# Optimization experiments

Hardware: AMD Instinct MI355X
Metric: run time of the kernel (lower is better)

Reference implementation:

```python
import jax, jax.numpy as jnp
from jax import lax
import numpy as np

B, S, D, H = 64, 512, 1024, 1024


def setup_inputs() -> dict:
    key = jax.random.key(0)
    ks = jax.random.split(key, 9)
    s = 1.0 / np.sqrt(H)
    return {
        "x": jax.random.normal(ks[0], (B, S, D), jnp.float32),
        "W_ih0": jax.random.normal(ks[1], (H, D), jnp.float32) * s,
        "b_ih0": jax.random.normal(ks[2], (H,), jnp.float32) * s,
        "W_hh0": jax.random.normal(ks[3], (H, H), jnp.float32) * s,
        "b_hh0": jax.random.normal(ks[4], (H,), jnp.float32) * s,
        "W_ih1": jax.random.normal(ks[5], (H, H), jnp.float32) * s,
        "b_ih1": jax.random.normal(ks[6], (H,), jnp.float32) * s,
        "W_hh1": jax.random.normal(ks[7], (H, H), jnp.float32) * s,
        "b_hh1": jax.random.normal(ks[8], (H,), jnp.float32) * s,
    }


def reference(x, W_ih0, b_ih0, W_hh0, b_hh0, W_ih1, b_ih1, W_hh1, b_hh1):
    batch = x.shape[0]
    hid = W_hh0.shape[0]
    params = [(W_ih0, b_ih0, W_hh0, b_hh0), (W_ih1, b_ih1, W_hh1, b_hh1)]
    h0 = jnp.zeros((len(params), batch, hid), x.dtype)

    def step(h, xt):
        # xt: [B, D]; h: [L, B, H]
        inp = xt
        new_h = []
        for l, (Wi, bi, Wh, bh) in enumerate(params):
            inp = jnp.tanh(inp @ Wi.T + bi + h[l] @ Wh.T + bh)
            new_h.append(inp)
        return jnp.stack(new_h), inp

    hT, outs = lax.scan(step, h0, jnp.swapaxes(x, 0, 1))  # outs: [S, B, H]
    return jnp.swapaxes(outs, 0, 1), hT
```

## Files before the change

### kernel.cpp

```cpp
#include <hip/hip_runtime.h>
#include <hip/hip_bf16.h>

#define RNN_B 64
#define RNN_S 512
#define RNN_H 1024
#define BH (RNN_B * RNN_H)
#define L0_NBLK 64
#define L1_NBLK 128
#define NBLK (L0_NBLK + L1_NBLK)
#define NFLAGS 192
#define FLAG_STRIDE 32
#define OUTS_ELEMS ((size_t)RNN_B * RNN_S * RNN_H)

typedef _Float16 f16;
typedef __attribute__((ext_vector_type(8))) _Float16 f16x8;
typedef __attribute__((ext_vector_type(8))) short bf16x8;
typedef __attribute__((ext_vector_type(4))) float f32x4;
typedef __attribute__((ext_vector_type(2))) float f32x2;
typedef __attribute__((ext_vector_type(4))) int i32x4;

__device__ f32x4 __rnn_rawbufload_x4(i32x4 srsrc, int voffset, int soffset,
                                     int cachepolicy) __asm("llvm.amdgcn.raw.buffer.load.v4f32");

__device__ __forceinline__ i32x4 make_srd(const void* p, unsigned bytes) {
  i32x4 r;
  r[0] = (int)(unsigned)(unsigned long long)p;
  r[1] = (int)((unsigned long long)p >> 32);
  r[2] = (int)bytes;
  r[3] = 0x00020000;
  return r;
}

__device__ __forceinline__ f16x8 ld_h(i32x4 srd, int byteoff) {
  union { f32x4 f; f16x8 h; } u;
  u.f = __rnn_rawbufload_x4(srd, byteoff, 0, 17);
  return u.h;
}

__device__ __forceinline__ void st_sys_u32(void* p, unsigned v) {
  asm volatile("global_store_dword %0, %1, off sc0 sc1" :: "v"(p), "v"(v) : "memory");
}
__device__ __forceinline__ void st_sys_u64(void* p, unsigned long long v) {
  asm volatile("global_store_dwordx2 %0, %1, off sc0 sc1" :: "v"(p), "v"(v) : "memory");
}

__device__ __forceinline__ unsigned pack2f16(float a, float b) {
  union { f16 h[2]; unsigned u; } v;
  v.h[0] = (f16)a; v.h[1] = (f16)b;
  return v.u;
}
__device__ __forceinline__ unsigned long long pack4f16(const float* f) {
  union { f16 h[4]; unsigned long long u; } v;
  #pragma unroll
  for (int i = 0; i < 4; ++i) v.h[i] = (f16)f[i];
  return v.u;
}

__device__ __forceinline__ short f2bf(float f) {
  union { float f; unsigned u; } v; v.f = f;
  return (short)((v.u + 0x7FFFu + ((v.u >> 16) & 1u)) >> 16);
}
__device__ __forceinline__ float bf2f(short h) {
  union { unsigned u; float f; } v; v.u = ((unsigned)(unsigned short)h) << 16;
  return v.f;
}
__device__ __forceinline__ f32x4 mfma16b(bf16x8 a, bf16x8 b, f32x4 c) {
  return __builtin_amdgcn_mfma_f32_16x16x32_bf16(a, b, c, 0, 0, 0);
}
__device__ __forceinline__ f32x4 mfma16f(f16x8 a, f16x8 b, f32x4 c) {
  return __builtin_amdgcn_mfma_f32_16x16x32_f16(a, b, c, 0, 0, 0);
}
__device__ __forceinline__ void cvt8_hl(const float* f, bf16x8* hi, bf16x8* lo) {
  #pragma unroll
  for (int i = 0; i < 8; ++i) {
    short h = f2bf(f[i]);
    (*hi)[i] = h;
    (*lo)[i] = f2bf(f[i] - bf2f(h));
  }
}
__device__ __forceinline__ f16x8 cvt8f(const float* f) {
  f16x8 r;
  #pragma unroll
  for (int i = 0; i < 8; ++i) r[i] = (f16)f[i];
  return r;
}

__global__ __launch_bounds__(256) void a0_gemm(
    const float* __restrict__ x, const float* __restrict__ Wih0,
    const float* __restrict__ bih0, const float* __restrict__ bhh0,
    float* __restrict__ A0, unsigned* __restrict__ flags)
{
  if (blockIdx.x == 0) {
    for (int i = threadIdx.x; i < NFLAGS * FLAG_STRIDE; i += 256)
      __hip_atomic_store(&flags[i], 0u, __ATOMIC_RELAXED, __HIP_MEMORY_SCOPE_SYSTEM);
  }
  const int bn = blockIdx.x & 7;
  const int bm = blockIdx.x >> 3;
  const int tid = threadIdx.x;
  const int lane = tid & 63;
  const int w = tid >> 6;
  const int wr = w >> 1, wc = w & 1;
  const int l15 = lane & 15, lq = lane >> 4;

  __shared__ short As[2][128][40];
  __shared__ short Bs[2][128][40];

  f32x4 acc[4][4] = {};

  const int sr = tid >> 1;
  const int sc = (tid & 1) << 4;
  const float* xp = x + (size_t)(bm * 128 + sr) * RNN_H + sc;
  const float* wp = Wih0 + (size_t)(bn * 128 + sr) * RNN_H + sc;

  for (int k0 = 0; k0 < RNN_H; k0 += 32) {
    float xa[16], wa[16];
    #pragma unroll
    for (int j = 0; j < 4; ++j) {
      *(float4*)&xa[j * 4] = *(const float4*)(xp + k0 + j * 4);
      *(float4*)&wa[j * 4] = *(const float4*)(wp + k0 + j * 4);
    }
    __syncthreads();
    bf16x8 h0, l0, h1, l1;
    cvt8_hl(&xa[0], &h0, &l0); cvt8_hl(&xa[8], &h1, &l1);
    *(bf16x8*)&As[0][sr][sc] = h0; *(bf16x8*)&As[1][sr][sc] = l0;
    *(bf16x8*)&As[0][sr][sc + 8] = h1; *(bf16x8*)&As[1][sr][sc + 8] = l1;
    cvt8_hl(&wa[0], &h0, &l0); cvt8_hl(&wa[8], &h1, &l1);
    *(bf16x8*)&Bs[0][sr][sc] = h0; *(bf16x8*)&Bs[1][sr][sc] = l0;
    *(bf16x8*)&Bs[0][sr][sc + 8] = h1; *(bf16x8*)&Bs[1][sr][sc + 8] = l1;
    __syncthreads();
    bf16x8 ah[4], al[4], bh[4], bl[4];
    #pragma unroll
    for (int i = 0; i < 4; ++i) {
      ah[i] = *(const bf16x8*)&As[0][wr * 64 + i * 16 + l15][lq * 8];
      al[i] = *(const bf16x8*)&As[1][wr * 64 + i * 16 + l15][lq * 8];
    }
    #pragma unroll
    for (int j = 0; j < 4; ++j) {
      bh[j] = *(const bf16x8*)&Bs[0][wc * 64 + j * 16 + l15][lq * 8];
      bl[j] = *(const bf16x8*)&Bs[1][wc * 64 + j * 16 + l15][lq * 8];
    }
    #pragma unroll
    for (int i = 0; i < 4; ++i)
      #pragma unroll
      for (int j = 0; j < 4; ++j) {
        acc[i][j] = mfma16b(ah[i], bh[j], acc[i][j]);
        acc[i][j] = mfma16b(al[i], bh[j], acc[i][j]);
        acc[i][j] = mfma16b(ah[i], bl[j], acc[i][j]);
      }
  }

  #pragma unroll
  for (int j = 0; j < 4; ++j) {
    const int col = bn * 128 + wc * 64 + j * 16 + l15;
    const float bias = bih0[col] + bhh0[col];
    #pragma unroll
    for (int i = 0; i < 4; ++i) {
      const int row0 = bm * 128 + wr * 64 + i * 16 + lq * 4;
      #pragma unroll
      for (int r = 0; r < 4; ++r)
        A0[(size_t)(row0 + r) * RNN_H + col] = acc[i][j][r] + bias;
    }
  }
}

__device__ __forceinline__ void waitflags(const unsigned* fbase, int tL0, int tL1) {
  if (threadIdx.x < 64) {
    const int l = threadIdx.x;
    const unsigned* f = fbase + (l < 48 ? l : 0) * FLAG_STRIDE;
    const int tgt = (l < 16) ? tL0 : (l < 48 ? tL1 : (-0x7FFFFFFF));
    while (!__all((int)__hip_atomic_load(f, __ATOMIC_RELAXED,
                                         __HIP_MEMORY_SCOPE_SYSTEM) >= tgt))
      __builtin_amdgcn_s_sleep(1);
  }
  __syncthreads();
}

__device__ __forceinline__ void publish(unsigned* slot, unsigned v) {
  asm volatile("s_waitcnt vmcnt(0)" ::: "memory");
  __syncthreads();
  if (threadIdx.x == 0)
    __hip_atomic_store(slot, v, __ATOMIC_RELAXED, __HIP_MEMORY_SCOPE_SYSTEM);
}

__global__ __launch_bounds__(256) void rnn_rec(
    const float* __restrict__ Whh0,
    const float* __restrict__ Wih1, const float* __restrict__ bih1,
    const float* __restrict__ Whh1, const float* __restrict__ bhh1,
    float* outs,
    f16* __restrict__ h0buf,
    f16* __restrict__ h1buf,
    unsigned* flags, int dmask)
{
  const int bid = blockIdx.x;
  const bool isL0 = bid < L0_NBLK;
  const int tid = threadIdx.x;
  const int w = tid >> 6;
  const int lane = tid & 63;
  const int l15 = lane & 15;
  const int lq = lane >> 4;
  const int swz = l15 & 7;
  const int dlag = dmask;

  int b0, n0, bs, cs;
  if (isL0) { bs = bid >> 4; cs = bid & 15; b0 = bs * 16; n0 = cs * 64; }
  else { const int b2 = bid - L0_NBLK; bs = b2 >> 5; cs = b2 & 31; b0 = bs * 16; n0 = cs * 32; }

  unsigned* fbase = flags + bs * 48 * FLAG_STRIDE;
  unsigned* myflag = fbase + (isL0 ? cs : 16 + cs) * FLAG_STRIDE;

  const unsigned HBYT = (unsigned)(dmask + 1) * BH * 2u;
  const i32x4 srd_h0 = make_srd(h0buf, HBYT);
  const i32x4 srd_h1 = make_srd(h1buf, HBYT);

  __shared__ __align__(16) f16 Ws[2 * 32 * RNN_H];
  __shared__ __align__(16) float red[4][16][64];

  if (isL0) {
    const int n = tid >> 2;
    const int kb = (tid & 3) * 256;
    const float* src = Whh0 + (size_t)(n0 + n) * RNN_H + kb;
    f16* dst = Ws + n * RNN_H;
    #pragma unroll 4
    for (int j = 0; j < 32; ++j) {
      float tmp[8];
      *(float4*)&tmp[0] = *(const float4*)(src + j * 8);
      *(float4*)&tmp[4] = *(const float4*)(src + j * 8 + 4);
      const int c = (kb >> 3) + j;
      *(f16x8*)&dst[((c ^ (n & 7)) << 3)] = cvt8f(tmp);
    }
  } else {
    const int n = tid >> 3;
    const int kb = (tid & 7) * 128;
    #pragma unroll
    for (int m = 0; m < 2; ++m) {
      const float* src = (m ? Whh1 : Wih1) + (size_t)(n0 + n) * RNN_H + kb;
      f16* dst = Ws + m * 32 * RNN_H + n * RNN_H;
      #pragma unroll 4
      for (int j = 0; j < 16; ++j) {
        float tmp[8];
        *(float4*)&tmp[0] = *(const float4*)(src + j * 8);
        *(float4*)&tmp[4] = *(const float4*)(src + j * 8 + 4);
        const int c = (kb >> 3) + j;
        *(f16x8*)&dst[((c ^ (n & 7)) << 3)] = cvt8f(tmp);
      }
    }
  }

  float* hT = outs + OUTS_ELEMS;

  const int crow = tid & 15;
  const int cg = tid >> 4;
  float bias1a = 0.f, bias1b = 0.f;
  if (!isL0) {
    bias1a = bih1[n0 + cg * 2]     + bhh1[n0 + cg * 2];
    bias1b = bih1[n0 + cg * 2 + 1] + bhh1[n0 + cg * 2 + 1];
  }
  __syncthreads();

  if (isL0) {
    f32x4 a0v = *(const f32x4*)&outs[((size_t)(b0 + crow) * RNN_S + 0) * RNN_H + n0 + cg * 4];

    for (int p = 0; p < RNN_S; ++p) {
      waitflags(fbase, p, p - dlag);
      if (p > 0) {
        const int hb = (((p - 1) & dmask) * BH + (b0 + l15) * RNN_H + w * 256 + lq * 8) * 2;
        f32x4 acc[4] = {};
        #pragma unroll
        for (int ks = 0; ks < 8; ++ks) {
          f16x8 hx = ld_h(srd_h0, hb + ks * 64);
          const int c = ((w * 32 + ks * 4 + lq) ^ swz) << 3;
          #pragma unroll
          for (int ct = 0; ct < 4; ++ct)
            acc[ct] = mfma16f(hx, *(const f16x8*)&Ws[(ct * 16 + l15) * RNN_H + c], acc[ct]);
        }
        #pragma unroll
        for (int ct = 0; ct < 4; ++ct)
          #pragma unroll
          for (int r = 0; r < 4; ++r)
            red[w][lq * 4 + r][ct * 16 + l15] = acc[ct][r];
      }
      __syncthreads();
      float vals[4];
      #pragma unroll
      for (int j = 0; j < 4; ++j) {
        float s = a0v[j];
        if (p > 0)
          s += red[0][crow][cg * 4 + j] + red[1][crow][cg * 4 + j]
             + red[2][crow][cg * 4 + j] + red[3][crow][cg * 4 + j];
        vals[j] = tanhf(s);
      }
      st_sys_u64(&h0buf[(size_t)(p & dmask) * BH + (size_t)(b0 + crow) * RNN_H + n0 + cg * 4],
                 pack4f16(vals));
      publish(myflag, (unsigned)(p + 1));
      if (p == RNN_S - 1) {
        f32x4 hv = { vals[0], vals[1], vals[2], vals[3] };
        *(f32x4*)&hT[(size_t)(b0 + crow) * RNN_H + n0 + cg * 4] = hv;
      }
      if (p + 1 < RNN_S)
        a0v = *(const f32x4*)&outs[((size_t)(b0 + crow) * RNN_S + (p + 1)) * RNN_H + n0 + cg * 4];
    }
  } else {
    for (int t = 0; t < RNN_S; ++t) {
      waitflags(fbase, t + 1, t);
      const int hb0 = ((t & dmask) * BH + (b0 + l15) * RNN_H + w * 256 + lq * 8) * 2;
      f32x4 acc[2] = {};
      if (t > 0) {
        const int hb1 = (((t - 1) & dmask) * BH + (b0 + l15) * RNN_H + w * 256 + lq * 8) * 2;
        #pragma unroll
        for (int ks = 0; ks < 8; ++ks) {
          f16x8 hx = ld_h(srd_h0, hb0 + ks * 64);
          f16x8 gx = ld_h(srd_h1, hb1 + ks * 64);
          const int c = ((w * 32 + ks * 4 + lq) ^ swz) << 3;
          #pragma unroll
          for (int ct = 0; ct < 2; ++ct) {
            acc[ct] = mfma16f(hx, *(const f16x8*)&Ws[(ct * 16 + l15) * RNN_H + c], acc[ct]);
            acc[ct] = mfma16f(gx, *(const f16x8*)&Ws[32 * RNN_H + (ct * 16 + l15) * RNN_H + c], acc[ct]);
          }
        }
      } else {
        #pragma unroll
        for (int ks = 0; ks < 8; ++ks) {
          f16x8 hx = ld_h(srd_h0, hb0 + ks * 64);
          const int c = ((w * 32 + ks * 4 + lq) ^ swz) << 3;
          #pragma unroll
          for (int ct = 0; ct < 2; ++ct)
            acc[ct] = mfma16f(hx, *(const f16x8*)&Ws[(ct * 16 + l15) * RNN_H + c], acc[ct]);
        }
      }
      #pragma unroll
      for (int ct = 0; ct < 2; ++ct)
        #pragma unroll
        for (int r = 0; r < 4; ++r)
          red[w][lq * 4 + r][ct * 16 + l15] = acc[ct][r];
      __syncthreads();
      float s0 = bias1a + red[0][crow][cg * 2]     + red[1][crow][cg * 2]
                        + red[2][crow][cg * 2]     + red[3][crow][cg * 2];
      float s1 = bias1b + red[0][crow][cg * 2 + 1] + red[1][crow][cg * 2 + 1]
                        + red[2][crow][cg * 2 + 1] + red[3][crow][cg * 2 + 1];
      const float v0 = tanhf(s0), v1 = tanhf(s1);
      st_sys_u32(&h1buf[(size_t)(t & dmask) * BH + (size_t)(b0 + crow) * RNN_H + n0 + cg * 2],
                 pack2f16(v0, v1));
      publish(myflag, (unsigned)(t + 1));
      {
        f32x2 ov = { v0, v1 };
        *(f32x2*)&outs[((size_t)(b0 + crow) * RNN_S + t) * RNN_H + n0 + cg * 2] = ov;
        if (t == RNN_S - 1)
          *(f32x2*)&hT[(size_t)BH + (size_t)(b0 + crow) * RNN_H + n0 + cg * 2] = ov;
      }
    }
  }
}

extern "C" void kernel_launch(void* const* d_in, const int* in_sizes, int n_in,
                              void* d_out, int out_size, void* d_ws, size_t ws_size,
                              hipStream_t stream) {
  const float* x    = (const float*)d_in[0];
  const float* Wih0 = (const float*)d_in[1];
  const float* bih0 = (const float*)d_in[2];
  const float* Whh0 = (const float*)d_in[3];
  const float* bhh0 = (const float*)d_in[4];
  const float* Wih1 = (const float*)d_in[5];
  const float* bih1 = (const float*)d_in[6];
  const float* Whh1 = (const float*)d_in[7];
  const float* bhh1 = (const float*)d_in[8];
  float* outs = (float*)d_out;

  const size_t flagBytes = 32768;
  const size_t need4 = flagBytes + 2 * (size_t)4 * BH * sizeof(f16);
  const int D = (ws_size >= need4) ? 4 : 2;
  unsigned* flags = (unsigned*)d_ws;
  f16* h0buf = (f16*)((char*)d_ws + flagBytes);
  f16* h1buf = h0buf + (size_t)D * BH;

  a0_gemm<<<2048, 256, 0, stream>>>(x, Wih0, bih0, bhh0, outs, flags);
  rnn_rec<<<NBLK, 256, 0, stream>>>(Whh0, Wih1, bih1, Whh1, bhh1, outs,
                                    h0buf, h1buf, flags, D - 1);
}
```

Before: 2.409 ms.

## Replace block-wide flag wait with per-wave waits on needed producers only

Each wave now polls only the flags of the L0 blocks producing its K-slice of h, plus the L1 flags, rather than having wave 0 poll all flags and then run a block-wide barrier. This removes one __syncthreads per step and lets waves begin their MFMA work as soon as their own inputs are ready. The reduction buffer row is padded from 64 to 68 floats, and the cross-wave reduction reads it as vectors, to cut LDS bank conflicts and load count. The risk is that the per-wave producer mapping (w*4+lane) has to match the K-slices each wave reads exactly, or correctness breaks.

```diff
diff --git a/kernel.cpp b/kernel.cpp
--- a/kernel.cpp
+++ b/kernel.cpp
@@ -163,23 +163,23 @@
   }
 }
 
-__device__ __forceinline__ void waitflags(const unsigned* fbase, int tL0, int tL1) {
-  if (threadIdx.x < 64) {
-    const int l = threadIdx.x;
-    const unsigned* f = fbase + (l < 48 ? l : 0) * FLAG_STRIDE;
-    const int tgt = (l < 16) ? tL0 : (l < 48 ? tL1 : (-0x7FFFFFFF));
-    while (!__all((int)__hip_atomic_load(f, __ATOMIC_RELAXED,
-                                         __HIP_MEMORY_SCOPE_SYSTEM) >= tgt))
-      __builtin_amdgcn_s_sleep(1);
-  }
-  __syncthreads();
-}
-
 __device__ __forceinline__ void publish(unsigned* slot, unsigned v) {
   asm volatile("s_waitcnt vmcnt(0)" ::: "memory");
   __syncthreads();
   if (threadIdx.x == 0)
     __hip_atomic_store(slot, v, __ATOMIC_RELAXED, __HIP_MEMORY_SCOPE_SYSTEM);
+}
+
+__device__ __forceinline__ void wavewait(const unsigned* fbase, int lane, int w,
+                                         int tProd, int tL1) {
+  const unsigned* f;
+  int tgt;
+  if (lane < 4)       { f = fbase + (w * 4 + lane) * FLAG_STRIDE; tgt = tProd; }
+  else if (lane < 36) { f = fbase + (12 + lane) * FLAG_STRIDE;    tgt = tL1;  }
+  else                { f = fbase;                                tgt = (int)0x80000000; }
+  while (!__all((int)__hip_atomic_load(f, __ATOMIC_RELAXED,
+                                       __HIP_MEMORY_SCOPE_SYSTEM) >= tgt))
+    __builtin_amdgcn_s_sleep(1);
 }
 
 __global__ __launch_bounds__(256) void rnn_rec(
@@ -213,7 +213,7 @@
   const i32x4 srd_h1 = make_srd(h1buf, HBYT);
 
   __shared__ __align__(16) f16 Ws[2 * 32 * RNN_H];
-  __shared__ __align__(16) float red[4][16][64];
+  __shared__ __align__(16) float red[4][16][68];
 
   if (isL0) {
     const int n = tid >> 2;
@@ -261,7 +261,7 @@
     f32x4 a0v = *(const f32x4*)&outs[((size_t)(b0 + crow) * RNN_S + 0) * RNN_H + n0 + cg * 4];
 
     for (int p = 0; p < RNN_S; ++p) {
-      waitflags(fbase, p, p - dlag);
+      wavewait(fbase, lane, w, p, p - dlag);
       if (p > 0) {
         const int hb = (((p - 1) & dmask) * BH + (b0 + l15) * RNN_H + w * 256 + lq * 8) * 2;
         f32x4 acc[4] = {};
@@ -280,15 +280,15 @@
             red[w][lq * 4 + r][ct * 16 + l15] = acc[ct][r];
       }
       __syncthreads();
+      f32x4 s4 = a0v;
+      if (p > 0) {
+        #pragma unroll
+        for (int ww = 0; ww < 4; ++ww)
+          s4 += *(const f32x4*)&red[ww][crow][cg * 4];
+      }
       float vals[4];
       #pragma unroll
-      for (int j = 0; j < 4; ++j) {
-        float s = a0v[j];
-        if (p > 0)
-          s += red[0][crow][cg * 4 + j] + red[1][crow][cg * 4 + j]
-             + red[2][crow][cg * 4 + j] + red[3][crow][cg * 4 + j];
-        vals[j] = tanhf(s);
-      }
+      for (int j = 0; j < 4; ++j) vals[j] = tanhf(s4[j]);
       st_sys_u64(&h0buf[(size_t)(p & dmask) * BH + (size_t)(b0 + crow) * RNN_H + n0 + cg * 4],
                  pack4f16(vals));
       publish(myflag, (unsigned)(p + 1));
@@ -301,7 +301,7 @@
     }
   } else {
     for (int t = 0; t < RNN_S; ++t) {
-      waitflags(fbase, t + 1, t);
+      wavewait(fbase, lane, w, t + 1, t);
       const int hb0 = ((t & dmask) * BH + (b0 + l15) * RNN_H + w * 256 + lq * 8) * 2;
       f32x4 acc[2] = {};
       if (t > 0) {
@@ -333,11 +333,11 @@
         for (int r = 0; r < 4; ++r)
           red[w][lq * 4 + r][ct * 16 + l15] = acc[ct][r];
       __syncthreads();
-      float s0 = bias1a + red[0][crow][cg * 2]     + red[1][crow][cg * 2]
-                        + red[2][crow][cg * 2]     + red[3][crow][cg * 2];
-      float s1 = bias1b + red[0][crow][cg * 2 + 1] + red[1][crow][cg * 2 + 1]
-                        + red[2][crow][cg * 2 + 1] + red[3][crow][cg * 2 + 1];
-      const float v0 = tanhf(s0), v1 = tanhf(s1);
+      f32x2 s2 = { bias1a, bias1b };
+      #pragma unroll
+      for (int ww = 0; ww < 4; ++ww)
+        s2 += *(const f32x2*)&red[ww][crow][cg * 2];
+      const float v0 = tanhf(s2[0]), v1 = tanhf(s2[1]);
       st_sys_u32(&h1buf[(size_t)(t & dmask) * BH + (size_t)(b0 + crow) * RNN_H + n0 + cg * 2],
                  pack2f16(v0, v1));
       publish(myflag, (unsigned)(t + 1));
```

Result: faster. 2.201 ms (-8.6%).
